# Optimization experiments

Hardware: AMD Instinct MI355X
Metric: run time of the kernel (lower is better)

The kernel has to match this reference:

```python
import jax, jax.numpy as jnp
import numpy as np

ALPHA = 1.0

def setup_inputs() -> dict:
    key = jax.random.key(0)
    kx, kc = jax.random.split(key)
    x = jax.random.normal(kx, (2048, 128, 32), dtype=jnp.float32)      # (N, T, F)
    clusters = jax.random.normal(kc, (32, 128, 32), dtype=jnp.float32)  # (K, T, F)
    return {"x": x, "clusters": clusters}

def reference(x, clusters):
    # Euclidean-over-time distance per feature:
    #   ed[n,k,f] = sqrt(sum_t (x[n,t,f] - c[k,t,f])^2)
    # computed via the expanded quadratic form to avoid the (N,K,T,F) broadcast.
    x2 = jnp.sum(x * x, axis=1)               # (N, F)
    c2 = jnp.sum(clusters * clusters, axis=1)  # (K, F)
    xc = jnp.einsum('ntf,ktf->nkf', x, clusters)  # (N, K, F)
    sq = x2[:, None, :] + c2[None, :, :] - 2.0 * xc
    ed = jnp.sqrt(jnp.maximum(sq, 0.0))        # (N, K, F)
    distance = jnp.sum(ed, axis=-1)            # (N, K)
    # Student's t soft assignment
    q = 1.0 / (1.0 + (distance * distance) / ALPHA)
    q = q ** ((ALPHA + 1.0) / 2.0)
    q = q / jnp.sum(q, axis=1, keepdims=True)
    return q
```

## Files before the change

### kernel.cpp

```cpp
#include <hip/hip_runtime.h>


#define T_DIM 128
#define F_DIM 32
#define K_DIM 32
#define TF (T_DIM * F_DIM)

__global__ __launch_bounds__(256, 1) void tscluster_kernel(
    const float* __restrict__ x,
    const float* __restrict__ c,
    float* __restrict__ out)
{
    const int tid   = threadIdx.x;
    const int f_grp = tid & 7;
    const int k_grp = (tid >> 3) & 7;
    const int n_grp = tid >> 6;
    const int f0 = f_grp << 2;
    const int k0 = k_grp << 2;
    const int n0 = (blockIdx.x << 3) + (n_grp << 1);

    const float* xp0 = x + (size_t)n0 * TF + f0;
    const float* xp1 = xp0 + TF;
    const float* cp0 = c + (size_t)k0 * TF + f0;
    const float* cp1 = cp0 + TF;
    const float* cp2 = cp1 + TF;
    const float* cp3 = cp2 + TF;

    float acc[2][4][4];
    #pragma unroll
    for (int a = 0; a < 2; ++a)
        #pragma unroll
        for (int b = 0; b < 4; ++b)
            #pragma unroll
            for (int j = 0; j < 4; ++j)
                acc[a][b][j] = 0.0f;

    #pragma unroll 2
    for (int t = 0; t < T_DIM; ++t) {
        const int off = t * F_DIM;
        const float4 xv0 = *reinterpret_cast<const float4*>(xp0 + off);
        const float4 xv1 = *reinterpret_cast<const float4*>(xp1 + off);
        const float4 cv0 = *reinterpret_cast<const float4*>(cp0 + off);
        const float4 cv1 = *reinterpret_cast<const float4*>(cp1 + off);
        const float4 cv2 = *reinterpret_cast<const float4*>(cp2 + off);
        const float4 cv3 = *reinterpret_cast<const float4*>(cp3 + off);

        const float xs0[4] = {xv0.x, xv0.y, xv0.z, xv0.w};
        const float xs1[4] = {xv1.x, xv1.y, xv1.z, xv1.w};
        const float cs[4][4] = {
            {cv0.x, cv0.y, cv0.z, cv0.w},
            {cv1.x, cv1.y, cv1.z, cv1.w},
            {cv2.x, cv2.y, cv2.z, cv2.w},
            {cv3.x, cv3.y, cv3.z, cv3.w},
        };

        #pragma unroll
        for (int kk = 0; kk < 4; ++kk) {
            #pragma unroll
            for (int j = 0; j < 4; ++j) {
                const float d0 = xs0[j] - cs[kk][j];
                acc[0][kk][j] += d0 * d0;
                const float d1 = xs1[j] - cs[kk][j];
                acc[1][kk][j] += d1 * d1;
            }
        }
    }

    float dist[2][4];
    #pragma unroll
    for (int a = 0; a < 2; ++a)
        #pragma unroll
        for (int b = 0; b < 4; ++b)
            dist[a][b] = sqrtf(acc[a][b][0]) + sqrtf(acc[a][b][1]) +
                         sqrtf(acc[a][b][2]) + sqrtf(acc[a][b][3]);

    #pragma unroll
    for (int off = 1; off < 8; off <<= 1) {
        #pragma unroll
        for (int a = 0; a < 2; ++a)
            #pragma unroll
            for (int b = 0; b < 4; ++b)
                dist[a][b] += __shfl_xor(dist[a][b], off, 64);
    }

    float qun[2][4];
    float qs[2];
    #pragma unroll
    for (int a = 0; a < 2; ++a) {
        qs[a] = 0.0f;
        #pragma unroll
        for (int b = 0; b < 4; ++b) {
            qun[a][b] = 1.0f / (1.0f + dist[a][b] * dist[a][b]);
            qs[a] += qun[a][b];
        }
    }

    #pragma unroll
    for (int off = 8; off < 64; off <<= 1) {
        #pragma unroll
        for (int a = 0; a < 2; ++a)
            qs[a] += __shfl_xor(qs[a], off, 64);
    }

    if (f_grp == 0) {
        #pragma unroll
        for (int a = 0; a < 2; ++a) {
            float4 qv;
            qv.x = qun[a][0] / qs[a];
            qv.y = qun[a][1] / qs[a];
            qv.z = qun[a][2] / qs[a];
            qv.w = qun[a][3] / qs[a];
            *reinterpret_cast<float4*>(out + (size_t)(n0 + a) * K_DIM + k0) = qv;
        }
    }
}

extern "C" void kernel_launch(void* const* d_in, const int* in_sizes, int n_in,
                              void* d_out, int out_size, void* d_ws, size_t ws_size,
                              hipStream_t stream) {
    const float* x = (const float*)d_in[0];
    const float* c = (const float*)d_in[1];
    float* out = (float*)d_out;
    tscluster_kernel<<<dim3(256), dim3(256), 0, stream>>>(x, c, out);
}
```

Baseline: 100.0 us.

## Split time dimension across eight waves with LDS reduction of partial sums

Each block now covers 4 samples with 512 threads, and each of the 8 waves accumulates squared differences over a 16-step slice of the time axis. The partial accumulators are then combined through shared memory in two stages before wave 0 does the sqrt, row sum and normalisation. The aim is many more waves in flight to hide global-load latency, plus more x reuse per thread (4 samples instead of 2). In exchange it adds two LDS round-trips of 64 floats per thread and several barriers. The tight launch bound (512 threads, 4 blocks) may force register spills of the 64-element accumulator.

After: 109.4 us. +9.4%, slower.

```diff
diff --git a/kernel.cpp b/kernel.cpp
--- a/kernel.cpp
+++ b/kernel.cpp
@@ -5,30 +5,33 @@
 #define F_DIM 32
 #define K_DIM 32
 #define TF (T_DIM * F_DIM)
+#define NB 4
+#define TS 8
+#define TT (T_DIM/TS)
+#define SLOT_STRIDE 65
 
-__global__ __launch_bounds__(256, 1) void tscluster_kernel(
+__global__ __launch_bounds__(512, 4) void tscluster_kernel(
     const float* __restrict__ x,
     const float* __restrict__ c,
     float* __restrict__ out)
 {
+    __shared__ float lds[4 * 64 * SLOT_STRIDE];
+
     const int tid   = threadIdx.x;
-    const int f_grp = tid & 7;
-    const int k_grp = (tid >> 3) & 7;
-    const int n_grp = tid >> 6;
+    const int lane  = tid & 63;
+    const int w     = tid >> 6;
+    const int f_grp = lane & 7;
+    const int k_grp = (lane >> 3) & 7;
     const int f0 = f_grp << 2;
     const int k0 = k_grp << 2;
-    const int n0 = (blockIdx.x << 3) + (n_grp << 1);
+    const int n0 = blockIdx.x * NB;
 
-    const float* xp0 = x + (size_t)n0 * TF + f0;
-    const float* xp1 = xp0 + TF;
-    const float* cp0 = c + (size_t)k0 * TF + f0;
-    const float* cp1 = cp0 + TF;
-    const float* cp2 = cp1 + TF;
-    const float* cp3 = cp2 + TF;
+    const float* xp = x + (size_t)n0 * TF + w * TT * F_DIM + f0;
+    const float* cp = c + (size_t)k0 * TF + w * TT * F_DIM + f0;
 
-    float acc[2][4][4];
+    float acc[NB][4][4];
     #pragma unroll
-    for (int a = 0; a < 2; ++a)
+    for (int a = 0; a < NB; ++a)
         #pragma unroll
         for (int b = 0; b < 4; ++b)
             #pragma unroll
@@ -36,81 +39,110 @@
                 acc[a][b][j] = 0.0f;
 
     #pragma unroll 2
-    for (int t = 0; t < T_DIM; ++t) {
-        const int off = t * F_DIM;
-        const float4 xv0 = *reinterpret_cast<const float4*>(xp0 + off);
-        const float4 xv1 = *reinterpret_cast<const float4*>(xp1 + off);
-        const float4 cv0 = *reinterpret_cast<const float4*>(cp0 + off);
-        const float4 cv1 = *reinterpret_cast<const float4*>(cp1 + off);
-        const float4 cv2 = *reinterpret_cast<const float4*>(cp2 + off);
-        const float4 cv3 = *reinterpret_cast<const float4*>(cp3 + off);
+    for (int tt = 0; tt < TT; ++tt) {
+        const int off = tt * F_DIM;
 
-        const float xs0[4] = {xv0.x, xv0.y, xv0.z, xv0.w};
-        const float xs1[4] = {xv1.x, xv1.y, xv1.z, xv1.w};
-        const float cs[4][4] = {
-            {cv0.x, cv0.y, cv0.z, cv0.w},
-            {cv1.x, cv1.y, cv1.z, cv1.w},
-            {cv2.x, cv2.y, cv2.z, cv2.w},
-            {cv3.x, cv3.y, cv3.z, cv3.w},
-        };
+        float4 xv[NB], cv[4];
+        #pragma unroll
+        for (int a = 0; a < NB; ++a)
+            xv[a] = *reinterpret_cast<const float4*>(xp + (size_t)a * TF + off);
+        #pragma unroll
+        for (int b = 0; b < 4; ++b)
+            cv[b] = *reinterpret_cast<const float4*>(cp + (size_t)b * TF + off);
+
+        float xs[NB][4], cs[4][4];
+        #pragma unroll
+        for (int a = 0; a < NB; ++a) {
+            xs[a][0] = xv[a].x; xs[a][1] = xv[a].y; xs[a][2] = xv[a].z; xs[a][3] = xv[a].w;
+        }
+        #pragma unroll
+        for (int b = 0; b < 4; ++b) {
+            cs[b][0] = cv[b].x; cs[b][1] = cv[b].y; cs[b][2] = cv[b].z; cs[b][3] = cv[b].w;
+        }
 
         #pragma unroll
-        for (int kk = 0; kk < 4; ++kk) {
+        for (int a = 0; a < NB; ++a)
             #pragma unroll
-            for (int j = 0; j < 4; ++j) {
-                const float d0 = xs0[j] - cs[kk][j];
-                acc[0][kk][j] += d0 * d0;
-                const float d1 = xs1[j] - cs[kk][j];
-                acc[1][kk][j] += d1 * d1;
+            for (int b = 0; b < 4; ++b)
+                #pragma unroll
+                for (int j = 0; j < 4; ++j) {
+                    const float d = xs[a][j] - cs[b][j];
+                    acc[a][b][j] += d * d;
+                }
+    }
+
+    float* accf = &acc[0][0][0];
+
+    if (w >= 4) {
+        float* dst = lds + ((size_t)(w - 4) * 64 + lane) * SLOT_STRIDE;
+        #pragma unroll
+        for (int i = 0; i < 64; ++i) dst[i] = accf[i];
+    }
+    __syncthreads();
+    if (w < 4) {
+        const float* src = lds + ((size_t)w * 64 + lane) * SLOT_STRIDE;
+        #pragma unroll
+        for (int i = 0; i < 64; ++i) accf[i] += src[i];
+    }
+    __syncthreads();
+    if (w >= 1 && w < 4) {
+        float* dst = lds + ((size_t)(w - 1) * 64 + lane) * SLOT_STRIDE;
+        #pragma unroll
+        for (int i = 0; i < 64; ++i) dst[i] = accf[i];
+    }
+    __syncthreads();
+
+    if (w == 0) {
+        #pragma unroll
+        for (int s = 0; s < 3; ++s) {
+            const float* src = lds + ((size_t)s * 64 + lane) * SLOT_STRIDE;
+            #pragma unroll
+            for (int i = 0; i < 64; ++i) accf[i] += src[i];
+        }
+
+        float dist[NB][4];
+        #pragma unroll
+        for (int a = 0; a < NB; ++a)
+            #pragma unroll
+            for (int b = 0; b < 4; ++b)
+                dist[a][b] = sqrtf(acc[a][b][0]) + sqrtf(acc[a][b][1]) +
+                             sqrtf(acc[a][b][2]) + sqrtf(acc[a][b][3]);
+
+        #pragma unroll
+        for (int off = 1; off < 8; off <<= 1)
+            #pragma unroll
+            for (int a = 0; a < NB; ++a)
+                #pragma unroll
+                for (int b = 0; b < 4; ++b)
+                    dist[a][b] += __shfl_xor(dist[a][b], off, 64);
+
+        float qun[NB][4], qs[NB];
+        #pragma unroll
+        for (int a = 0; a < NB; ++a) {
+            qs[a] = 0.0f;
+            #pragma unroll
+            for (int b = 0; b < 4; ++b) {
+                qun[a][b] = 1.0f / (1.0f + dist[a][b] * dist[a][b]);
+                qs[a] += qun[a][b];
             }
         }
-    }
 
-    float dist[2][4];
-    #pragma unroll
-    for (int a = 0; a < 2; ++a)
         #pragma unroll
-        for (int b = 0; b < 4; ++b)
-            dist[a][b] = sqrtf(acc[a][b][0]) + sqrtf(acc[a][b][1]) +
-                         sqrtf(acc[a][b][2]) + sqrtf(acc[a][b][3]);
+        for (int off = 8; off < 64; off <<= 1)
+            #pragma unroll
+            for (int a = 0; a < NB; ++a)
+                qs[a] += __shfl_xor(qs[a], off, 64);
 
-    #pragma unroll
-    for (int off = 1; off < 8; off <<= 1) {
-        #pragma unroll
-        for (int a = 0; a < 2; ++a)
+        if (f_grp == 0) {
             #pragma unroll
-            for (int b = 0; b < 4; ++b)
-                dist[a][b] += __shfl_xor(dist[a][b], off, 64);
-    }
-
-    float qun[2][4];
-    float qs[2];
-    #pragma unroll
-    for (int a = 0; a < 2; ++a) {
-        qs[a] = 0.0f;
-        #pragma unroll
-        for (int b = 0; b < 4; ++b) {
-            qun[a][b] = 1.0f / (1.0f + dist[a][b] * dist[a][b]);
-            qs[a] += qun[a][b];
-        }
-    }
-
-    #pragma unroll
-    for (int off = 8; off < 64; off <<= 1) {
-        #pragma unroll
-        for (int a = 0; a < 2; ++a)
-            qs[a] += __shfl_xor(qs[a], off, 64);
-    }
-
-    if (f_grp == 0) {
-        #pragma unroll
-        for (int a = 0; a < 2; ++a) {
-            float4 qv;
-            qv.x = qun[a][0] / qs[a];
-            qv.y = qun[a][1] / qs[a];
-            qv.z = qun[a][2] / qs[a];
-            qv.w = qun[a][3] / qs[a];
-            *reinterpret_cast<float4*>(out + (size_t)(n0 + a) * K_DIM + k0) = qv;
+            for (int a = 0; a < NB; ++a) {
+                float4 qv;
+                qv.x = qun[a][0] / qs[a];
+                qv.y = qun[a][1] / qs[a];
+                qv.z = qun[a][2] / qs[a];
+                qv.w = qun[a][3] / qs[a];
+                *reinterpret_cast<float4*>(out + (size_t)(n0 + a) * K_DIM + k0) = qv;
+            }
         }
     }
 }
@@ -121,5 +153,5 @@
     const float* x = (const float*)d_in[0];
     const float* c = (const float*)d_in[1];
     float* out = (float*)d_out;
-    tscluster_kernel<<<dim3(256), dim3(256), 0, stream>>>(x, c, out);
+    tscluster_kernel<<<dim3(2048 / NB), dim3(512), 0, stream>>>(x, c, out);
 }
```
